# Optimization experiments

Measured on AMD Instinct MI355X. Metric: run time of the kernel, lower is better.

The kernel has to match this reference:

```python
import jax, jax.numpy as jnp
import numpy as np

EPS = 1e-12  # F.normalize eps

def _l2norm(v, axis):
    n = jnp.sqrt(jnp.sum(v * v, axis=axis, keepdims=True))
    return v / jnp.maximum(n, EPS)

def setup_inputs() -> dict:
    key = jax.random.key(0)
    ks = jax.random.split(key, 4)
    B, N, C, centers = 128, 196, 768, 64
    x = jax.random.normal(ks[0], (B, N, C), dtype=jnp.float32)
    k_c = jax.random.normal(ks[1], (C, centers), dtype=jnp.float32)
    v_c = jax.random.normal(ks[2], (centers, N, N), dtype=jnp.float32)
    proj_w = jax.random.normal(ks[3], (C, C), dtype=jnp.float32) * (C ** -0.5)
    proj_b = jnp.zeros((C,), dtype=jnp.float32)
    return {"x": x, "k_c": k_c, "v_c": v_c, "proj_w": proj_w, "proj_b": proj_b}

def reference(x, k_c, v_c, proj_w, proj_b):
    # x: (B, N, C); k_c: (C, centers); v_c: (centers, N, N)
    C = x.shape[-1]
    scale = C ** -0.5
    q = x.mean(axis=1)                                  # (B, C)
    attn = _l2norm(q, -1) @ _l2norm(k_c, 0)             # (B, centers)
    attn = jax.nn.softmax(attn * scale, axis=-1)        # (B, centers)
    # attention-weighted mixture of basis matrices: (B,centers)x(centers,N*N) GEMM
    v = jnp.einsum('bc,cnm->bnm', attn, v_c)            # (B, N, N)
    out = jnp.einsum('bnm,bmd->bnd', v, x)              # (B, N, C)
    out = out @ proj_w.T + proj_b                        # Linear(dim, dim)
    return out
```

## Files before the change

kernel.cpp:

```cpp
#include <hip/hip_runtime.h>
#include <hip/hip_bf16.h>


#define NB   128
#define NN   196
#define NC   768
#define NCEN 64
#define RPAD 256
#define KPAD 224
#define BGRP 32

using bf16x8 = __attribute__((ext_vector_type(8))) short;
using f32x4  = __attribute__((ext_vector_type(4))) float;

__device__ __forceinline__ void async_copy16(const void* g, void* l) {
    __builtin_amdgcn_global_load_lds((const __attribute__((address_space(1))) void*)g,
                                     (__attribute__((address_space(3))) void*)l, 16, 0, 0);
}

__global__ __launch_bounds__(256)
void convert_x_kernel(const float* __restrict__ x, __hip_bfloat16* __restrict__ x_bf,
                      float* __restrict__ q_part) {
    int b = blockIdx.x, chunk = blockIdx.y, part = blockIdx.z, t = threadIdx.x;
    int c = chunk * 256 + t;
    const float* xp = x + (size_t)b * NN * NC + c;
    __hip_bfloat16* xo = x_bf + (size_t)b * RPAD * NC + c;
    float s = 0.f;
    int m0 = part * 64;
#pragma unroll 4
    for (int m = m0; m < m0 + 64; ++m) {
        if (m < NN) {
            float v = xp[(size_t)m * NC];
            s += v;
            xo[(size_t)m * NC] = __float2bfloat16(v);
        } else {
            xo[(size_t)m * NC] = __float2bfloat16(0.f);
        }
    }
    q_part[((size_t)part * NB + b) * NC + c] = s;
}

__global__ __launch_bounds__(256)
void convert_w_kernel(const float* __restrict__ w, __hip_bfloat16* __restrict__ w_bf) {
    int i = blockIdx.x * 256 + threadIdx.x;
    if (i < NC * NC) w_bf[i] = __float2bfloat16(w[i]);
}

__global__ __launch_bounds__(256)
void attn_kernel(const float* __restrict__ q_part, const float* __restrict__ k_c,
                 float* __restrict__ attn) {
    const float SCALE = 0.03608439182435161f;
    int b = blockIdx.x, t = threadIdx.x;
    __shared__ float qs[NC];
    __shared__ float red[256];
    __shared__ float pd[4][NCEN];
    __shared__ float pk[4][NCEN];

    const size_t PS = (size_t)NB * NC;
    for (int i = t; i < NC; i += 256) {
        size_t idx = (size_t)b * NC + i;
        qs[i] = (q_part[idx] + q_part[PS + idx] + q_part[2 * PS + idx] + q_part[3 * PS + idx])
                * (1.0f / (float)NN);
    }
    __syncthreads();

    float s = 0.f;
    for (int i = t; i < NC; i += 256) { float v = qs[i]; s += v * v; }
    red[t] = s;
    __syncthreads();
    for (int o = 128; o > 0; o >>= 1) {
        if (t < o) red[t] += red[t + o];
        __syncthreads();
    }
    float qn = sqrtf(red[0]);

    int j = t & 63, part = t >> 6;
    float d = 0.f, kk = 0.f;
    int c0 = part * 192;
    for (int c = c0; c < c0 + 192; ++c) {
        float kv = k_c[c * NCEN + j];
        d += kv * qs[c];
        kk += kv * kv;
    }
    pd[part][j] = d;
    pk[part][j] = kk;
    __syncthreads();

    if (t < NCEN) {
        float dot = pd[0][t] + pd[1][t] + pd[2][t] + pd[3][t];
        float kn  = sqrtf(pk[0][t] + pk[1][t] + pk[2][t] + pk[3][t]);
        float lg = dot / (fmaxf(qn, 1e-12f) * fmaxf(kn, 1e-12f)) * SCALE;
        float mx = lg;
        for (int o = 32; o > 0; o >>= 1) mx = fmaxf(mx, __shfl_xor(mx, o, 64));
        float e = expf(lg - mx);
        float sum = e;
        for (int o = 32; o > 0; o >>= 1) sum += __shfl_xor(sum, o, 64);
        attn[b * NCEN + t] = e / sum;
    }
}

__global__ __launch_bounds__(256)
void mix_kernel(const float* __restrict__ attn, const float* __restrict__ v_c,
                __hip_bfloat16* __restrict__ v_pad) {
    int n = blockIdx.x;
    int g = blockIdx.y;
    int m = threadIdx.x;

    __shared__ float sattn[BGRP][NCEN];
    for (int i = threadIdx.x; i < BGRP * NCEN; i += 256)
        sattn[i >> 6][i & 63] = attn[(g * BGRP + (i >> 6)) * NCEN + (i & 63)];
    __syncthreads();

    if (m >= KPAD) return;
    __hip_bfloat16 z = __float2bfloat16(0.f);
    size_t base = (size_t)n * KPAD + m;
    if (n >= NN || m >= NN) {
#pragma unroll
        for (int bb = 0; bb < BGRP; ++bb)
            v_pad[(size_t)(g * BGRP + bb) * RPAD * KPAD + base] = z;
        return;
    }
    float vc[NCEN];
    const float* vp = v_c + (size_t)n * NN + m;
#pragma unroll
    for (int c = 0; c < NCEN; ++c) vc[c] = vp[(size_t)c * NN * NN];
#pragma unroll
    for (int bb = 0; bb < BGRP; ++bb) {
        float acc = 0.f;
#pragma unroll
        for (int c = 0; c < NCEN; ++c) acc += sattn[bb][c] * vc[c];
        v_pad[(size_t)(g * BGRP + bb) * RPAD * KPAD + base] = __float2bfloat16(acc);
    }
}

template <int BK, bool OUT_BF16>
__global__ __launch_bounds__(256)
void gemm_nt(const __hip_bfloat16* __restrict__ A, size_t strideA,
             const __hip_bfloat16* __restrict__ Bm, size_t strideB,
             void* __restrict__ Cout, size_t strideC,
             const float* __restrict__ bias,
             int lda, int ldb, int ldc, int K, int Mstore, int Nstore) {
    int bm = blockIdx.x, bn = blockIdx.y, bb = blockIdx.z;
    const unsigned short* Ab = (const unsigned short*)A + (size_t)bb * strideA + (size_t)bm * 128 * lda;
    const unsigned short* Bb = (const unsigned short*)Bm + (size_t)bb * strideB + (size_t)bn * 128 * ldb;

    __shared__ __align__(16) unsigned short sA[128 * BK];
    __shared__ __align__(16) unsigned short sB[128 * BK];

    int tid = threadIdx.x;
    int wave = tid >> 6, lane = tid & 63;
    int wr = wave >> 1, wc = wave & 1;
    int lrow = lane & 15, quad = lane >> 4;

    constexpr int CH  = BK / 8;
    constexpr int RPI = 64 / CH;
    constexpr int NI  = 32 / RPI;
    int srow = lane / CH;
    int sc   = lane % CH;
    int lc   = (BK == 64) ? (sc ^ (srow & 7)) : sc;

    const unsigned short* ga[NI];
    const unsigned short* gb[NI];
    unsigned short* la[NI];
    unsigned short* lb[NI];
#pragma unroll
    for (int i = 0; i < NI; ++i) {
        int row = wave * 32 + i * RPI + srow;
        ga[i] = Ab + (size_t)row * lda + lc * 8;
        gb[i] = Bb + (size_t)row * ldb + lc * 8;
        la[i] = &sA[(wave * 32 + i * RPI) * BK];
        lb[i] = &sB[(wave * 32 + i * RPI) * BK];
    }

    f32x4 acc[4][4] = {};

    for (int k0 = 0; k0 < K; k0 += BK) {
        __syncthreads();
#pragma unroll
        for (int i = 0; i < NI; ++i) async_copy16(ga[i] + k0, la[i]);
#pragma unroll
        for (int i = 0; i < NI; ++i) async_copy16(gb[i] + k0, lb[i]);
        __syncthreads();

#pragma unroll
        for (int kh = 0; kh < BK / 32; ++kh) {
            int pcbase = (BK == 64) ? ((kh * 4 + quad) ^ (lrow & 7)) : quad;
            bf16x8 af[4], bfr[4];
#pragma unroll
            for (int i = 0; i < 4; ++i)
                af[i] = *(const bf16x8*)(&sA[(wr * 64 + i * 16 + lrow) * BK + pcbase * 8]);
#pragma unroll
            for (int j = 0; j < 4; ++j)
                bfr[j] = *(const bf16x8*)(&sB[(wc * 64 + j * 16 + lrow) * BK + pcbase * 8]);
#pragma unroll
            for (int i = 0; i < 4; ++i)
#pragma unroll
                for (int j = 0; j < 4; ++j)
                    acc[i][j] = __builtin_amdgcn_mfma_f32_16x16x32_bf16(af[i], bfr[j], acc[i][j], 0, 0, 0);
        }
    }

    size_t cbase = (size_t)bb * strideC;
#pragma unroll
    for (int i = 0; i < 4; ++i) {
        int row0 = bm * 128 + wr * 64 + i * 16 + quad * 4;
#pragma unroll
        for (int j = 0; j < 4; ++j) {
            int col = bn * 128 + wc * 64 + j * 16 + lrow;
            if (col < Nstore) {
                float badd = bias ? bias[col] : 0.f;
#pragma unroll
                for (int r = 0; r < 4; ++r) {
                    int row = row0 + r;
                    if (row < Mstore) {
                        float v = acc[i][j][r] + badd;
                        if (OUT_BF16)
                            ((__hip_bfloat16*)Cout)[cbase + (size_t)row * ldc + col] = __float2bfloat16(v);
                        else
                            ((float*)Cout)[cbase + (size_t)row * ldc + col] = v;
                    }
                }
            }
        }
    }
}

extern "C" void kernel_launch(void* const* d_in, const int* in_sizes, int n_in,
                              void* d_out, int out_size, void* d_ws, size_t ws_size,
                              hipStream_t stream) {
    const float* x      = (const float*)d_in[0];
    const float* k_c    = (const float*)d_in[1];
    const float* v_c    = (const float*)d_in[2];
    const float* proj_w = (const float*)d_in[3];
    const float* proj_b = (const float*)d_in[4];
    float* out = (float*)d_out;

    char* ws = (char*)d_ws;
    size_t off = 0;
    auto alloc = [&](size_t bytes) {
        void* p = ws + off;
        off = (off + bytes + 255) & ~(size_t)255;
        return p;
    };
    __hip_bfloat16* x_bf  = (__hip_bfloat16*)alloc((size_t)NB * RPAD * NC * 2);
    __hip_bfloat16* w_bf  = (__hip_bfloat16*)alloc((size_t)NC * NC * 2);
    __hip_bfloat16* xp_t  = (__hip_bfloat16*)alloc((size_t)NB * NC * KPAD * 2);
    __hip_bfloat16* v_pad = (__hip_bfloat16*)alloc((size_t)NB * RPAD * KPAD * 2);
    float* q_part = (float*)alloc((size_t)4 * NB * NC * 4);
    float* attn   = (float*)alloc((size_t)NB * NCEN * 4);

    convert_x_kernel<<<dim3(NB, 3, 4), 256, 0, stream>>>(x, x_bf, q_part);
    convert_w_kernel<<<dim3((NC * NC + 255) / 256), 256, 0, stream>>>(proj_w, w_bf);
    attn_kernel<<<dim3(NB), 256, 0, stream>>>(q_part, k_c, attn);
    mix_kernel<<<dim3(RPAD, NB / BGRP), 256, 0, stream>>>(attn, v_c, v_pad);

    gemm_nt<64, true><<<dim3(6, 2, NB), 256, 0, stream>>>(
        w_bf, 0, x_bf, (size_t)RPAD * NC, xp_t, (size_t)NC * KPAD, nullptr,
        NC, NC, KPAD, NC, NC, KPAD);

    gemm_nt<32, false><<<dim3(2, 6, NB), 256, 0, stream>>>(
        v_pad, (size_t)RPAD * KPAD, xp_t, (size_t)NC * KPAD, out, (size_t)NN * NC, proj_b,
        KPAD, KPAD, NC, KPAD, NN, NC);
}
```

Measured before the change: 320.0 us.

## Vectorize bf16 conversion kernels and remap GEMM blocks per XCD by batch

The x conversion kernel now handles 8 channels per thread with float4 loads and 16-byte bf16 stores. It splits rows into 7 parts with an in-block two-way reduction of partial column sums through shared memory, and attn_kernel sums 7 partials instead of 4. The weight conversion is vectorized the same way. Both GEMMs move to a 1D grid that assigns all tiles of one batch to the same XCD (blockIdx & 7), so tiles that share A/B operands hit a common L2. The trade-off is more partial-sum traffic and index arithmetic, plus a mapping that assumes 8-way round-robin XCD dispatch.

```diff
diff --git a/kernel.cpp b/kernel.cpp
--- a/kernel.cpp
+++ b/kernel.cpp
@@ -9,6 +9,7 @@
 #define RPAD 256
 #define KPAD 224
 #define BGRP 32
+#define QPARTS 7
 
 using bf16x8 = __attribute__((ext_vector_type(8))) short;
 using f32x4  = __attribute__((ext_vector_type(4))) float;
@@ -18,32 +19,71 @@
                                      (__attribute__((address_space(3))) void*)l, 16, 0, 0);
 }
 
-__global__ __launch_bounds__(256)
+__global__ __launch_bounds__(192)
 void convert_x_kernel(const float* __restrict__ x, __hip_bfloat16* __restrict__ x_bf,
                       float* __restrict__ q_part) {
-    int b = blockIdx.x, chunk = blockIdx.y, part = blockIdx.z, t = threadIdx.x;
-    int c = chunk * 256 + t;
+    __shared__ float qsh[NC];
+    int b = blockIdx.x, y = blockIdx.y, t = threadIdx.x;
+    int cg = t % 96, rg = t / 96;
+    int c = cg * 8;
     const float* xp = x + (size_t)b * NN * NC + c;
     __hip_bfloat16* xo = x_bf + (size_t)b * RPAD * NC + c;
-    float s = 0.f;
-    int m0 = part * 64;
-#pragma unroll 4
-    for (int m = m0; m < m0 + 64; ++m) {
-        if (m < NN) {
-            float v = xp[(size_t)m * NC];
-            s += v;
-            xo[(size_t)m * NC] = __float2bfloat16(v);
-        } else {
-            xo[(size_t)m * NC] = __float2bfloat16(0.f);
-        }
-    }
-    q_part[((size_t)part * NB + b) * NC + c] = s;
+    float s[8] = {0.f, 0.f, 0.f, 0.f, 0.f, 0.f, 0.f, 0.f};
+    int m0 = y * 28 + rg * 14;
+#pragma unroll 2
+    for (int m = m0; m < m0 + 14; ++m) {
+        const float* src = xp + (size_t)m * NC;
+        float4 v0 = *(const float4*)src;
+        float4 v1 = *(const float4*)(src + 4);
+        union { bf16x8 v; __hip_bfloat16 h[8]; } u;
+        u.h[0] = __float2bfloat16(v0.x); s[0] += v0.x;
+        u.h[1] = __float2bfloat16(v0.y); s[1] += v0.y;
+        u.h[2] = __float2bfloat16(v0.z); s[2] += v0.z;
+        u.h[3] = __float2bfloat16(v0.w); s[3] += v0.w;
+        u.h[4] = __float2bfloat16(v1.x); s[4] += v1.x;
+        u.h[5] = __float2bfloat16(v1.y); s[5] += v1.y;
+        u.h[6] = __float2bfloat16(v1.z); s[6] += v1.z;
+        u.h[7] = __float2bfloat16(v1.w); s[7] += v1.w;
+        *(bf16x8*)(xo + (size_t)m * NC) = u.v;
+    }
+    if (y == 6) {
+        bf16x8 z = {};
+        int mz0 = 196 + rg * 14;
+        for (int m = mz0; m < mz0 + 14; ++m)
+            *(bf16x8*)(xo + (size_t)m * NC) = z;
+    }
+    if (rg == 0) {
+#pragma unroll
+        for (int j = 0; j < 8; ++j) qsh[c + j] = s[j];
+    }
+    __syncthreads();
+    if (rg == 1) {
+        float* qp = q_part + ((size_t)y * NB + b) * NC + c;
+        float4 o0 = make_float4(qsh[c] + s[0], qsh[c + 1] + s[1],
+                                qsh[c + 2] + s[2], qsh[c + 3] + s[3]);
+        float4 o1 = make_float4(qsh[c + 4] + s[4], qsh[c + 5] + s[5],
+                                qsh[c + 6] + s[6], qsh[c + 7] + s[7]);
+        *(float4*)qp = o0;
+        *(float4*)(qp + 4) = o1;
+    }
 }
 
 __global__ __launch_bounds__(256)
 void convert_w_kernel(const float* __restrict__ w, __hip_bfloat16* __restrict__ w_bf) {
-    int i = blockIdx.x * 256 + threadIdx.x;
-    if (i < NC * NC) w_bf[i] = __float2bfloat16(w[i]);
+    int i = (blockIdx.x * 256 + threadIdx.x) * 8;
+    if (i >= NC * NC) return;
+    float4 v0 = *(const float4*)(w + i);
+    float4 v1 = *(const float4*)(w + i + 4);
+    union { bf16x8 v; __hip_bfloat16 h[8]; } u;
+    u.h[0] = __float2bfloat16(v0.x);
+    u.h[1] = __float2bfloat16(v0.y);
+    u.h[2] = __float2bfloat16(v0.z);
+    u.h[3] = __float2bfloat16(v0.w);
+    u.h[4] = __float2bfloat16(v1.x);
+    u.h[5] = __float2bfloat16(v1.y);
+    u.h[6] = __float2bfloat16(v1.z);
+    u.h[7] = __float2bfloat16(v1.w);
+    *(bf16x8*)(w_bf + i) = u.v;
 }
 
 __global__ __launch_bounds__(256)
@@ -59,8 +99,10 @@
     const size_t PS = (size_t)NB * NC;
     for (int i = t; i < NC; i += 256) {
         size_t idx = (size_t)b * NC + i;
-        qs[i] = (q_part[idx] + q_part[PS + idx] + q_part[2 * PS + idx] + q_part[3 * PS + idx])
-                * (1.0f / (float)NN);
+        float acc = 0.f;
+#pragma unroll
+        for (int p = 0; p < QPARTS; ++p) acc += q_part[p * PS + idx];
+        qs[i] = acc * (1.0f / (float)NN);
     }
     __syncthreads();
 
@@ -133,14 +175,23 @@
     }
 }
 
-template <int BK, bool OUT_BF16>
+template <int BK, bool OUT_BF16, int NBM, int NBN>
 __global__ __launch_bounds__(256)
 void gemm_nt(const __hip_bfloat16* __restrict__ A, size_t strideA,
              const __hip_bfloat16* __restrict__ Bm, size_t strideB,
              void* __restrict__ Cout, size_t strideC,
              const float* __restrict__ bias,
              int lda, int ldb, int ldc, int K, int Mstore, int Nstore) {
-    int bm = blockIdx.x, bn = blockIdx.y, bb = blockIdx.z;
+    constexpr int MPG = NBM * NBN;
+    int L = blockIdx.x;
+    int xcd = L & 7;
+    int r = L >> 3;
+    int q = r / MPG;
+    int i5 = r - q * MPG;
+    int bb = xcd + 8 * q;
+    int bm = i5 % NBM;
+    int bn = i5 / NBM;
+
     const unsigned short* Ab = (const unsigned short*)A + (size_t)bb * strideA + (size_t)bm * 128 * lda;
     const unsigned short* Bb = (const unsigned short*)Bm + (size_t)bb * strideB + (size_t)bn * 128 * ldb;
 
@@ -210,10 +261,10 @@
             if (col < Nstore) {
                 float badd = bias ? bias[col] : 0.f;
 #pragma unroll
-                for (int r = 0; r < 4; ++r) {
-                    int row = row0 + r;
+                for (int r2 = 0; r2 < 4; ++r2) {
+                    int row = row0 + r2;
                     if (row < Mstore) {
-                        float v = acc[i][j][r] + badd;
+                        float v = acc[i][j][r2] + badd;
                         if (OUT_BF16)
                             ((__hip_bfloat16*)Cout)[cbase + (size_t)row * ldc + col] = __float2bfloat16(v);
                         else
@@ -246,19 +297,19 @@
     __hip_bfloat16* w_bf  = (__hip_bfloat16*)alloc((size_t)NC * NC * 2);
     __hip_bfloat16* xp_t  = (__hip_bfloat16*)alloc((size_t)NB * NC * KPAD * 2);
     __hip_bfloat16* v_pad = (__hip_bfloat16*)alloc((size_t)NB * RPAD * KPAD * 2);
-    float* q_part = (float*)alloc((size_t)4 * NB * NC * 4);
+    float* q_part = (float*)alloc((size_t)QPARTS * NB * NC * 4);
     float* attn   = (float*)alloc((size_t)NB * NCEN * 4);
 
-    convert_x_kernel<<<dim3(NB, 3, 4), 256, 0, stream>>>(x, x_bf, q_part);
-    convert_w_kernel<<<dim3((NC * NC + 255) / 256), 256, 0, stream>>>(proj_w, w_bf);
+    convert_x_kernel<<<dim3(NB, 7), 192, 0, stream>>>(x, x_bf, q_part);
+    convert_w_kernel<<<dim3((NC * NC / 8 + 255) / 256), 256, 0, stream>>>(proj_w, w_bf);
     attn_kernel<<<dim3(NB), 256, 0, stream>>>(q_part, k_c, attn);
     mix_kernel<<<dim3(RPAD, NB / BGRP), 256, 0, stream>>>(attn, v_c, v_pad);
 
-    gemm_nt<64, true><<<dim3(6, 2, NB), 256, 0, stream>>>(
+    gemm_nt<64, true, 6, 2><<<dim3(6 * 2 * NB), 256, 0, stream>>>(
         w_bf, 0, x_bf, (size_t)RPAD * NC, xp_t, (size_t)NC * KPAD, nullptr,
         NC, NC, KPAD, NC, NC, KPAD);
 
-    gemm_nt<32, false><<<dim3(2, 6, NB), 256, 0, stream>>>(
+    gemm_nt<32, false, 2, 6><<<dim3(2 * 6 * NB), 256, 0, stream>>>(
         v_pad, (size_t)RPAD * KPAD, xp_t, (size_t)NC * KPAD, out, (size_t)NN * NC, proj_b,
         KPAD, KPAD, NC, KPAD, NN, NC);
 }
```

After: 289.1 us. 9.7% less time.
